# Optimization experiments

Hardware: AMD Instinct MI355X
Metric: run time of the kernel (lower is better)

The kernel has to match this reference:

```python
import jax, jax.numpy as jnp
import numpy as np

B, S, H = 2, 1024, 4544
NH, HD = 71, 64          # 71 query heads, head_dim 64, 1 shared kv head (multi-query)
THETA = 10000.0
NEG_INF = -1e9


def setup_inputs() -> dict:
    key = jax.random.key(0)
    k1, k2, k3 = jax.random.split(key, 3)
    hidden_states = jax.random.normal(k1, (B, S, H), dtype=jnp.float32)
    W_qkv = jax.random.normal(k2, (H, H + 2 * HD), dtype=jnp.float32) * 0.02
    W_dense = jax.random.normal(k3, (H, H), dtype=jnp.float32) * 0.02
    causal = jnp.tril(jnp.ones((S, S), dtype=bool))
    attention_mask = jnp.where(causal, 0.0, NEG_INF).astype(jnp.float32)[None, None]  # [1,1,S,S]
    position_ids = jnp.arange(S, dtype=jnp.int32)[None]  # [1,S]
    return {"hidden_states": hidden_states, "W_qkv": W_qkv, "W_dense": W_dense,
            "attention_mask": attention_mask, "position_ids": position_ids}


def _rope_cos_sin(position_ids):
    # HF FalconRotaryEmbedding: inv_freq over even dims, emb = cat(freqs, freqs)
    inv_freq = 1.0 / (THETA ** (jnp.arange(0, HD, 2, dtype=jnp.float32) / HD))
    freqs = position_ids.astype(jnp.float32)[..., None] * inv_freq  # [1,S,HD/2]
    emb = jnp.concatenate([freqs, freqs], axis=-1)                  # [1,S,HD]
    return jnp.cos(emb)[:, None], jnp.sin(emb)[:, None]             # [1,1,S,HD]


def _rotate_half(x):
    return jnp.concatenate([-x[..., HD // 2:], x[..., :HD // 2]], axis=-1)


def reference(hidden_states, W_qkv, W_dense, attention_mask, position_ids):
    # fused QKV projection (bias=False for Falcon-7B)
    fused = hidden_states @ W_qkv                       # [B,S,(NH+2)*HD]
    fused = fused.reshape(B, S, NH + 2, HD)
    q = jnp.transpose(fused[:, :, :NH], (0, 2, 1, 3))          # [B,NH,S,HD]
    k = jnp.transpose(fused[:, :, NH:NH + 1], (0, 2, 1, 3))    # [B,1,S,HD]
    v = jnp.transpose(fused[:, :, NH + 1:], (0, 2, 1, 3))      # [B,1,S,HD]

    cos, sin = _rope_cos_sin(position_ids)
    q = q * cos + _rotate_half(q) * sin
    k = k * cos + _rotate_half(k) * sin

    # scores: shared kv head broadcasts across the 71 query heads
    scores = jnp.matmul(q, jnp.swapaxes(k, -1, -2)) * (1.0 / np.sqrt(HD))  # [B,NH,S,S]
    probs = jax.nn.softmax(scores + attention_mask, axis=-1)
    attn = jnp.matmul(probs, v)                                            # [B,NH,S,HD]

    attn = jnp.transpose(attn, (0, 2, 1, 3)).reshape(B, S, NH * HD)
    return attn @ W_dense
```

## Files before the change

kernel.cpp:

```cpp
#include <hip/hip_runtime.h>

typedef unsigned short u16;
using f32x4  = __attribute__((ext_vector_type(4))) float;
using f32x16 = __attribute__((ext_vector_type(16))) float;
using s16x8  = __attribute__((ext_vector_type(8))) short;

static __device__ __forceinline__ u16 f2b(float f) {
  unsigned int u = __builtin_bit_cast(unsigned int, f);
  u = (u + 0x7fffu + ((u >> 16) & 1u)) >> 16;
  return (u16)u;
}
static __device__ __forceinline__ float b2f(u16 h) {
  unsigned int u = ((unsigned int)h) << 16;
  return __builtin_bit_cast(float, u);
}
static __device__ __forceinline__ unsigned int cvtpk(float lo, float hi) {
  unsigned int r;
  asm("v_cvt_pk_bf16_f32 %0, %1, %2" : "=v"(r) : "v"(lo), "v"(hi));
  return r;
}
static __device__ __forceinline__ void gload16(const void* g, void* l) {
  __builtin_amdgcn_global_load_lds(
      (const __attribute__((address_space(1))) void*)g,
      (__attribute__((address_space(3))) void*)l, 16, 0, 0);
}

__global__ __launch_bounds__(256) void conv_bf16(
    const float* __restrict__ in, u16* __restrict__ out, int n8)
{
  int i = blockIdx.x * 256 + threadIdx.x;
  if (i >= n8) return;
  float4 a = *(const float4*)(in + (size_t)i * 8);
  float4 b = *(const float4*)(in + (size_t)i * 8 + 4);
  __align__(16) u16 tmp[8] = {f2b(a.x), f2b(a.y), f2b(a.z), f2b(a.w),
                              f2b(b.x), f2b(b.y), f2b(b.z), f2b(b.w)};
  *(uint4*)(out + (size_t)i * 8) = *(const uint4*)tmp;
}

__global__ __launch_bounds__(256) void transpose_conv(
    const float* __restrict__ W, u16* __restrict__ Wt, int K, int N)
{
  __shared__ u16 tile[64][72];
  const int t = threadIdx.x;
  const int n0 = blockIdx.x * 64, k0 = blockIdx.y * 64;
  #pragma unroll
  for (int i = 0; i < 4; ++i) {
    int idx = i * 256 + t;
    int r = idx >> 4;
    int c = (idx & 15) << 2;
    float4 v = make_float4(0.f, 0.f, 0.f, 0.f);
    if (n0 + c < N) v = *(const float4*)(W + (size_t)(k0 + r) * N + n0 + c);
    tile[r][c + 0] = f2b(v.x);
    tile[r][c + 1] = f2b(v.y);
    tile[r][c + 2] = f2b(v.z);
    tile[r][c + 3] = f2b(v.w);
  }
  __syncthreads();
  #pragma unroll
  for (int i = 0; i < 2; ++i) {
    int idx = i * 256 + t;
    int rn = idx >> 3;
    int c8 = (idx & 7) << 3;
    __align__(16) u16 tmp[8];
    #pragma unroll
    for (int j = 0; j < 8; ++j) tmp[j] = tile[c8 + j][rn];
    *(uint4*)(Wt + (size_t)(n0 + rn) * K + k0 + c8) = *(const uint4*)tmp;
  }
}

template<bool OUT_BF16>
__global__ __launch_bounds__(256) void gemm_bt(
    const u16* __restrict__ A, const u16* __restrict__ B,
    void* __restrict__ Cptr, int M, int N, int K)
{
  __shared__ __align__(16) u16 aLds[128 * 32];
  __shared__ __align__(16) u16 bLds[128 * 32];

  const int t = threadIdx.x, lane = t & 63, w = t >> 6;
  const int lr = lane & 15, lg = lane >> 4;
  const int wr = w >> 1, wc = w & 1;
  const int m0 = blockIdx.y * 128, n0 = blockIdx.x * 128;

  const int srow = lane >> 2;
  const int skc  = (lane & 3) << 3;

  f32x4 acc[4][4] = {};

  const int nk = K >> 5;
  for (int kt = 0; kt < nk; ++kt) {
    const int k0 = kt << 5;
    __syncthreads();
    #pragma unroll
    for (int i = 0; i < 2; ++i) {
      int row = i * 64 + w * 16 + srow;
      gload16(A + (size_t)(m0 + row) * K + k0 + skc,
              (char*)aLds + i * 4096 + w * 1024);
      gload16(B + (size_t)(n0 + row) * K + k0 + skc,
              (char*)bLds + i * 4096 + w * 1024);
    }
    __syncthreads();
    s16x8 af[4], bf[4];
    #pragma unroll
    for (int m = 0; m < 4; ++m)
      af[m] = *(const s16x8*)(aLds + (wr * 64 + m * 16 + lr) * 32 + lg * 8);
    #pragma unroll
    for (int n = 0; n < 4; ++n)
      bf[n] = *(const s16x8*)(bLds + (wc * 64 + n * 16 + lr) * 32 + lg * 8);
    #pragma unroll
    for (int m = 0; m < 4; ++m)
      #pragma unroll
      for (int n = 0; n < 4; ++n)
        acc[m][n] = __builtin_amdgcn_mfma_f32_16x16x32_bf16(af[m], bf[n], acc[m][n], 0, 0, 0);
  }

  #pragma unroll
  for (int m = 0; m < 4; ++m) {
    int row = m0 + wr * 64 + m * 16 + lg * 4;
    #pragma unroll
    for (int n = 0; n < 4; ++n) {
      int col = n0 + wc * 64 + n * 16 + lr;
      if (col < N) {
        #pragma unroll
        for (int r = 0; r < 4; ++r) {
          if constexpr (OUT_BF16)
            ((u16*)Cptr)[(size_t)(row + r) * N + col] = f2b(acc[m][n][r]);
          else
            ((float*)Cptr)[(size_t)(row + r) * N + col] = acc[m][n][r];
        }
      }
    }
  }
}

__global__ __launch_bounds__(256) void rope_extract(
    const u16* __restrict__ fused, const int* __restrict__ pos_ids,
    u16* __restrict__ q, u16* __restrict__ kx, u16* __restrict__ vT)
{
  const int t   = threadIdx.x;
  const int row = blockIdx.x * 4 + (t >> 6);
  const int d   = t & 63;
  const int b   = row >> 10, s = row & 1023;
  const float p = (float)pos_ids[s];
  const float inv = exp2f(-0.41524101186092029f * (float)(d & 31));
  float sn, cs;
  sincosf(p * inv, &sn, &cs);
  const float sgn = (d < 32) ? -1.f : 1.f;
  const int dp = (d + 32) & 63;
  const u16* base = fused + (size_t)row * 4672;

  for (int h = 0; h < 71; ++h) {
    float x  = b2f(base[h * 64 + d]);
    float xp = b2f(base[h * 64 + dp]);
    q[((size_t)(b * 71 + h) * 1024 + s) * 64 + d] = f2b(x * cs + sgn * xp * sn);
  }
  {
    float x  = b2f(base[71 * 64 + d]);
    float xp = b2f(base[71 * 64 + dp]);
    kx[((size_t)b * 1024 + s) * 64 + d] = f2b(x * cs + sgn * xp * sn);
  }
  vT[((size_t)b * 64 + d) * 1024 + s] = base[72 * 64 + d];
}

__global__ __launch_bounds__(128) void attn_kernel(
    const u16* __restrict__ q, const u16* __restrict__ kx,
    const u16* __restrict__ vT, u16* __restrict__ attnO)
{
  const int t = threadIdx.x, lane = t & 63, w = t >> 6;
  const int lq  = lane & 31;
  const int hi  = lane >> 5;
  const int hi4 = hi << 2;
  const int pair = blockIdx.x, h = blockIdx.y, b = blockIdx.z;
  const int qt = w ? (31 - pair) : pair;
  const int q0 = qt * 32;

  const u16* qbase = q + ((size_t)(b * 71 + h) * 1024 + q0 + lq) * 64 + hi * 8;
  s16x8 qf[4];
  #pragma unroll
  for (int kt = 0; kt < 4; ++kt) qf[kt] = *(const s16x8*)(qbase + kt * 16);

  f32x16 o0 = {}, o1 = {};
  float m = -1e30f, l = 0.f;

  const u16* kbase  = kx + ((size_t)b * 1024 + lq) * 64 + hi * 8;
  const u16* vbase0 = vT + ((size_t)b * 64 + lq) * 1024 + hi * 8;
  const u16* vbase1 = vbase0 + 32 * 1024;

  for (int it = 0; it <= qt; ++it) {
    const int kv0 = it * 32;
    s16x8 kf[4];
    #pragma unroll
    for (int kt = 0; kt < 4; ++kt)
      kf[kt] = *(const s16x8*)(kbase + (size_t)kv0 * 64 + kt * 16);
    s16x8 v00 = *(const s16x8*)(vbase0 + kv0);
    s16x8 v01 = *(const s16x8*)(vbase0 + kv0 + 16);
    s16x8 v10 = *(const s16x8*)(vbase1 + kv0);
    s16x8 v11 = *(const s16x8*)(vbase1 + kv0 + 16);

    f32x16 sa = {}, sb = {};
    sa = __builtin_amdgcn_mfma_f32_32x32x16_bf16(kf[0], qf[0], sa, 0, 0, 0);
    sb = __builtin_amdgcn_mfma_f32_32x32x16_bf16(kf[1], qf[1], sb, 0, 0, 0);
    sa = __builtin_amdgcn_mfma_f32_32x32x16_bf16(kf[2], qf[2], sa, 0, 0, 0);
    sb = __builtin_amdgcn_mfma_f32_32x32x16_bf16(kf[3], qf[3], sb, 0, 0, 0);

    float s[16];
    float pmax = -1e30f;
    if (it == qt) {
      #pragma unroll
      for (int r = 0; r < 16; ++r) {
        int R = (r & 3) + ((r >> 2) << 3) + hi4;
        s[r] = (R > lq) ? -1e30f : (sa[r] + sb[r]) * 0.125f;
        pmax = fmaxf(pmax, s[r]);
      }
    } else {
      #pragma unroll
      for (int r = 0; r < 16; ++r) {
        s[r] = (sa[r] + sb[r]) * 0.125f;
        pmax = fmaxf(pmax, s[r]);
      }
    }
    pmax = fmaxf(pmax, __shfl_xor(pmax, 32));

    if (!__all(pmax <= m + 8.f)) {
      float mn = fmaxf(m, pmax);
      float corr = __expf(m - mn);
      m = mn;
      l *= corr;
      #pragma unroll
      for (int r = 0; r < 16; ++r) {
        float c2 = __shfl(corr, (r & 3) + ((r >> 2) << 3) + hi4);
        o0[r] *= c2; o1[r] *= c2;
      }
    }

    float p[16], sum = 0.f;
    #pragma unroll
    for (int r = 0; r < 16; ++r) { p[r] = __expf(s[r] - m); sum += p[r]; }
    sum += __shfl_xor(sum, 32);
    l += sum;

    unsigned int a0 = cvtpk(p[0], p[1]),   a1 = cvtpk(p[2], p[3]);
    unsigned int b0 = cvtpk(p[4], p[5]),   b1 = cvtpk(p[6], p[7]);
    asm("v_permlane32_swap_b32 %0, %1" : "+v"(a0), "+v"(b0));
    asm("v_permlane32_swap_b32 %0, %1" : "+v"(a1), "+v"(b1));
    unsigned int c0 = cvtpk(p[8], p[9]),   c1 = cvtpk(p[10], p[11]);
    unsigned int d0 = cvtpk(p[12], p[13]), d1 = cvtpk(p[14], p[15]);
    asm("v_permlane32_swap_b32 %0, %1" : "+v"(c0), "+v"(d0));
    asm("v_permlane32_swap_b32 %0, %1" : "+v"(c1), "+v"(d1));
    union { unsigned int wd[4]; s16x8 v; } palo, pahi;
    palo.wd[0] = a0; palo.wd[1] = a1; palo.wd[2] = b0; palo.wd[3] = b1;
    pahi.wd[0] = c0; pahi.wd[1] = c1; pahi.wd[2] = d0; pahi.wd[3] = d1;

    o0 = __builtin_amdgcn_mfma_f32_32x32x16_bf16(palo.v, v00, o0, 0, 0, 0);
    o0 = __builtin_amdgcn_mfma_f32_32x32x16_bf16(pahi.v, v01, o0, 0, 0, 0);
    o1 = __builtin_amdgcn_mfma_f32_32x32x16_bf16(palo.v, v10, o1, 0, 0, 0);
    o1 = __builtin_amdgcn_mfma_f32_32x32x16_bf16(pahi.v, v11, o1, 0, 0, 0);
  }

  float linv = 1.f / l;
  #pragma unroll
  for (int r = 0; r < 16; ++r) {
    int R = (r & 3) + ((r >> 2) << 3) + hi4;
    float c2 = __shfl(linv, R);
    size_t base = ((size_t)(b * 1024 + q0 + R) * 71 + h) * 64;
    attnO[base + lq]      = f2b(o0[r] * c2);
    attnO[base + 32 + lq] = f2b(o1[r] * c2);
  }
}

extern "C" void kernel_launch(void* const* d_in, const int* in_sizes, int n_in,
                              void* d_out, int out_size, void* d_ws, size_t ws_size,
                              hipStream_t stream) {
  const float* hidden = (const float*)d_in[0];
  const float* Wqkv   = (const float*)d_in[1];
  const float* Wdense = (const float*)d_in[2];
  const int*   pos    = (const int*)d_in[4];
  float* out = (float*)d_out;

  char* wsp = (char*)d_ws;
  u16* Wt    = (u16*)(wsp);
  u16* A1    = (u16*)(wsp + 43040768);
  u16* fused = (u16*)(wsp + 43040768 + 18612224);
  u16* kws   = (u16*)(wsp + 43040768 + 18612224 + 19136512);
  u16* vws   = (u16*)(wsp + 43040768 + 18612224 + 19136512 + 262144);
  u16* qws   = A1;
  u16* attnw = fused;

  conv_bf16<<<4544, 256, 0, stream>>>(hidden, A1, 2048 * 4544 / 8);
  transpose_conv<<<dim3(74, 71), 256, 0, stream>>>(Wqkv, Wt, 4544, 4672);
  gemm_bt<true><<<dim3(37, 16), 256, 0, stream>>>(A1, Wt, fused, 2048, 4672, 4544);
  rope_extract<<<512, 256, 0, stream>>>(fused, pos, qws, kws, vws);
  transpose_conv<<<dim3(72, 71), 256, 0, stream>>>(Wdense, Wt, 4544, 4544);
  attn_kernel<<<dim3(16, 71, 2), 128, 0, stream>>>(qws, kws, vws, attnw);
  gemm_bt<false><<<dim3(36, 16), 256, 0, stream>>>(attnw, Wt, out, 2048, 4544, 4544);
}
```

Before: 462.1 us.

## Replace GEMM with 256x256 double-buffered, pipelined MFMA kernel with block swizzle

Replaces the 128x128 single-buffered GEMM with a 256x256-tile, 512-thread kernel. It uses double-buffered LDS with 64-wide K steps, prefetches the next stage with global_load_lds, interleaves barriers and s_setprio around MFMA groups, and remaps block IDs with an XCD-style swizzle. The goal is more operand reuse per tile and overlap of memory loads with compute in both projection GEMMs. The risks are higher register and LDS pressure, a small grid (152/144 blocks) that may not cover all CUs, and a larger padded weight buffer.

```diff
diff --git a/kernel.cpp b/kernel.cpp
--- a/kernel.cpp
+++ b/kernel.cpp
@@ -69,53 +69,106 @@
 }
 
 template<bool OUT_BF16>
-__global__ __launch_bounds__(256) void gemm_bt(
+__global__ __launch_bounds__(512, 2) void gemm256(
     const u16* __restrict__ A, const u16* __restrict__ B,
-    void* __restrict__ Cptr, int M, int N, int K)
-{
-  __shared__ __align__(16) u16 aLds[128 * 32];
-  __shared__ __align__(16) u16 bLds[128 * 32];
+    void* __restrict__ Cptr, int M, int N, int K, int NB)
+{
+  __shared__ __align__(16) u16 sA[2][2][256 * 32];
+  __shared__ __align__(16) u16 sB[2][2][256 * 32];
 
   const int t = threadIdx.x, lane = t & 63, w = t >> 6;
   const int lr = lane & 15, lg = lane >> 4;
-  const int wr = w >> 1, wc = w & 1;
-  const int m0 = blockIdx.y * 128, n0 = blockIdx.x * 128;
-
-  const int srow = lane >> 2;
+  const int wr = w >> 2, wc = w & 3;
+
+  int bid = blockIdx.x;
+  int q = gridDim.x >> 3;
+  int swz = (bid & 7) * q + (bid >> 3);
+  const int m0 = (swz / NB) * 256, n0 = (swz % NB) * 256;
+
+  const int srow = w * 32 + (lane >> 2);
   const int skc  = (lane & 3) << 3;
-
-  f32x4 acc[4][4] = {};
-
-  const int nk = K >> 5;
+  const u16* Ast = A + (size_t)(m0 + srow) * K + skc;
+  const u16* Bst = B + (size_t)(n0 + srow) * K + skc;
+  const int ldsoff = w * 2048;
+
+  f32x4 acc[8][4] = {};
+  const int nk = K >> 6;
+
+#define STAGEU(tt, ks) do {                                                   \
+    int bp_ = (tt) & 1; size_t kc_ = (size_t)(tt) * 64 + (size_t)(ks) * 32;   \
+    gload16(Ast + kc_,                 (char*)&sA[bp_][ks][0] + ldsoff);      \
+    gload16(Ast + kc_ + 16 * (size_t)K,(char*)&sA[bp_][ks][0] + ldsoff+1024); \
+    gload16(Bst + kc_,                 (char*)&sB[bp_][ks][0] + ldsoff);      \
+    gload16(Bst + kc_ + 16 * (size_t)K,(char*)&sB[bp_][ks][0] + ldsoff+1024); \
+  } while (0)
+
+#define LOADA(rh, ks, cur) do {                                               \
+    const u16* ap_ = &sA[cur][ks][0] + ((wr*128 + (rh)*64 + lr) * 32) + lg*8; \
+    af[0] = *(const s16x8*)(ap_);                                             \
+    af[1] = *(const s16x8*)(ap_ + 16*32);                                     \
+    af[2] = *(const s16x8*)(ap_ + 32*32);                                     \
+    af[3] = *(const s16x8*)(ap_ + 48*32);                                     \
+  } while (0)
+
+#define LOADB(ks, cur) do {                                                   \
+    const u16* bp2_ = &sB[cur][ks][0] + ((wc*64 + lr) * 32) + lg*8;           \
+    bf[0] = *(const s16x8*)(bp2_);                                            \
+    bf[1] = *(const s16x8*)(bp2_ + 16*32);                                    \
+    bf[2] = *(const s16x8*)(bp2_ + 32*32);                                    \
+    bf[3] = *(const s16x8*)(bp2_ + 48*32);                                    \
+  } while (0)
+
+#define MFMAQ(rh) do {                                                        \
+    __builtin_amdgcn_s_setprio(1);                                            \
+    _Pragma("unroll")                                                         \
+    for (int m_ = 0; m_ < 4; ++m_)                                            \
+      _Pragma("unroll")                                                       \
+      for (int n_ = 0; n_ < 4; ++n_)                                          \
+        acc[(rh)*4 + m_][n_] = __builtin_amdgcn_mfma_f32_16x16x32_bf16(       \
+            af[m_], bf[n_], acc[(rh)*4 + m_][n_], 0, 0, 0);                   \
+    __builtin_amdgcn_s_setprio(0);                                            \
+  } while (0)
+
+  STAGEU(0, 0);
+  STAGEU(0, 1);
+  if (nk > 1) STAGEU(1, 0);
+  asm volatile("s_waitcnt vmcnt(8)" ::: "memory");
+  __builtin_amdgcn_s_barrier();
+
   for (int kt = 0; kt < nk; ++kt) {
-    const int k0 = kt << 5;
-    __syncthreads();
-    #pragma unroll
-    for (int i = 0; i < 2; ++i) {
-      int row = i * 64 + w * 16 + srow;
-      gload16(A + (size_t)(m0 + row) * K + k0 + skc,
-              (char*)aLds + i * 4096 + w * 1024);
-      gload16(B + (size_t)(n0 + row) * K + k0 + skc,
-              (char*)bLds + i * 4096 + w * 1024);
-    }
-    __syncthreads();
+    const int cur = kt & 1;
     s16x8 af[4], bf[4];
-    #pragma unroll
-    for (int m = 0; m < 4; ++m)
-      af[m] = *(const s16x8*)(aLds + (wr * 64 + m * 16 + lr) * 32 + lg * 8);
-    #pragma unroll
-    for (int n = 0; n < 4; ++n)
-      bf[n] = *(const s16x8*)(bLds + (wc * 64 + n * 16 + lr) * 32 + lg * 8);
-    #pragma unroll
-    for (int m = 0; m < 4; ++m)
-      #pragma unroll
-      for (int n = 0; n < 4; ++n)
-        acc[m][n] = __builtin_amdgcn_mfma_f32_16x16x32_bf16(af[m], bf[n], acc[m][n], 0, 0, 0);
-  }
-
-  #pragma unroll
-  for (int m = 0; m < 4; ++m) {
-    int row = m0 + wr * 64 + m * 16 + lg * 4;
+    if (kt + 1 < nk) STAGEU(kt + 1, 1);
+    LOADA(0, 0, cur); LOADB(0, cur);
+    __builtin_amdgcn_s_barrier();
+    MFMAQ(0);
+    __builtin_amdgcn_s_barrier();
+    LOADA(1, 0, cur);
+    __builtin_amdgcn_s_barrier();
+    MFMAQ(1);
+    if (kt + 1 < nk) asm volatile("s_waitcnt vmcnt(8)" ::: "memory");
+    else             asm volatile("s_waitcnt vmcnt(0)" ::: "memory");
+    __builtin_amdgcn_s_barrier();
+    if (kt + 2 < nk) STAGEU(kt + 2, 0);
+    LOADA(0, 1, cur); LOADB(1, cur);
+    __builtin_amdgcn_s_barrier();
+    MFMAQ(0);
+    __builtin_amdgcn_s_barrier();
+    LOADA(1, 1, cur);
+    __builtin_amdgcn_s_barrier();
+    MFMAQ(1);
+    if (kt + 2 < nk)      asm volatile("s_waitcnt vmcnt(8)" ::: "memory");
+    else if (kt + 1 < nk) asm volatile("s_waitcnt vmcnt(4)" ::: "memory");
+    __builtin_amdgcn_s_barrier();
+  }
+#undef STAGEU
+#undef LOADA
+#undef LOADB
+#undef MFMAQ
+
+  #pragma unroll
+  for (int mm = 0; mm < 8; ++mm) {
+    int row = m0 + wr * 128 + (mm >> 2) * 64 + (mm & 3) * 16 + lg * 4;
     #pragma unroll
     for (int n = 0; n < 4; ++n) {
       int col = n0 + wc * 64 + n * 16 + lr;
@@ -123,9 +176,9 @@
         #pragma unroll
         for (int r = 0; r < 4; ++r) {
           if constexpr (OUT_BF16)
-            ((u16*)Cptr)[(size_t)(row + r) * N + col] = f2b(acc[m][n][r]);
+            ((u16*)Cptr)[(size_t)(row + r) * N + col] = f2b(acc[mm][n][r]);
           else
-            ((float*)Cptr)[(size_t)(row + r) * N + col] = acc[m][n][r];
+            ((float*)Cptr)[(size_t)(row + r) * N + col] = acc[mm][n][r];
         }
       }
     }
@@ -278,18 +331,18 @@
 
   char* wsp = (char*)d_ws;
   u16* Wt    = (u16*)(wsp);
-  u16* A1    = (u16*)(wsp + 43040768);
-  u16* fused = (u16*)(wsp + 43040768 + 18612224);
-  u16* kws   = (u16*)(wsp + 43040768 + 18612224 + 19136512);
-  u16* vws   = (u16*)(wsp + 43040768 + 18612224 + 19136512 + 262144);
+  u16* A1    = (u16*)(wsp + 44208128);
+  u16* fused = (u16*)(wsp + 44208128 + 18612224);
+  u16* kws   = (u16*)(wsp + 44208128 + 18612224 + 19136512);
+  u16* vws   = (u16*)(wsp + 44208128 + 18612224 + 19136512 + 262144);
   u16* qws   = A1;
   u16* attnw = fused;
 
   conv_bf16<<<4544, 256, 0, stream>>>(hidden, A1, 2048 * 4544 / 8);
-  transpose_conv<<<dim3(74, 71), 256, 0, stream>>>(Wqkv, Wt, 4544, 4672);
-  gemm_bt<true><<<dim3(37, 16), 256, 0, stream>>>(A1, Wt, fused, 2048, 4672, 4544);
+  transpose_conv<<<dim3(76, 71), 256, 0, stream>>>(Wqkv, Wt, 4544, 4672);
+  gemm256<true><<<152, 512, 0, stream>>>(A1, Wt, fused, 2048, 4672, 4544, 19);
   rope_extract<<<512, 256, 0, stream>>>(fused, pos, qws, kws, vws);
   transpose_conv<<<dim3(72, 71), 256, 0, stream>>>(Wdense, Wt, 4544, 4544);
   attn_kernel<<<dim3(16, 71, 2), 128, 0, stream>>>(qws, kws, vws, attnw);
-  gemm_bt<false><<<dim3(36, 16), 256, 0, stream>>>(attnw, Wt, out, 2048, 4544, 4544);
-}
+  gemm256<false><<<144, 512, 0, stream>>>(attnw, Wt, out, 2048, 4544, 4544, 18);
+}
```

Result: slower. 565.4 us (+22.3%).

## Fuse RoPE and Q/K/V extraction into QKV GEMM epilogue, swizzle block order

Applied to the files above, without the earlier changes.

Drops the separate rope_extract kernel. The QKV GEMM epilogue now applies rotary embedding directly from the fp32 accumulators and writes q, k and transposed v in their final layouts, so the bf16 fused intermediate is never written and re-read. Both GEMMs also switch to a 1D grid with a block-index swizzle meant to improve L2 reuse of A/B tiles. The trade-off is a heavier epilogue with scattered 2-byte stores (especially the strided vT writes) and fast __sincosf, which is less accurate than sincosf.

```diff
diff --git a/kernel.cpp b/kernel.cpp
--- a/kernel.cpp
+++ b/kernel.cpp
@@ -68,10 +68,13 @@
   }
 }
 
-template<bool OUT_BF16>
+template<int MODE>
 __global__ __launch_bounds__(256) void gemm_bt(
     const u16* __restrict__ A, const u16* __restrict__ B,
-    void* __restrict__ Cptr, int M, int N, int K)
+    float* __restrict__ Cptr,
+    u16* __restrict__ qo, u16* __restrict__ ko, u16* __restrict__ vo,
+    const int* __restrict__ pos,
+    int M, int N, int K, int NBX)
 {
   __shared__ __align__(16) u16 aLds[128 * 32];
   __shared__ __align__(16) u16 bLds[128 * 32];
@@ -79,7 +82,11 @@
   const int t = threadIdx.x, lane = t & 63, w = t >> 6;
   const int lr = lane & 15, lg = lane >> 4;
   const int wr = w >> 1, wc = w & 1;
-  const int m0 = blockIdx.y * 128, n0 = blockIdx.x * 128;
+
+  const int bid = blockIdx.x;
+  const int qq  = gridDim.x >> 3;
+  const int swz = (bid & 7) * qq + (bid >> 3);
+  const int m0 = (swz / NBX) * 128, n0 = (swz % NBX) * 128;
 
   const int srow = lane >> 2;
   const int skc  = (lane & 3) << 3;
@@ -113,52 +120,58 @@
         acc[m][n] = __builtin_amdgcn_mfma_f32_16x16x32_bf16(af[m], bf[n], acc[m][n], 0, 0, 0);
   }
 
-  #pragma unroll
-  for (int m = 0; m < 4; ++m) {
-    int row = m0 + wr * 64 + m * 16 + lg * 4;
-    #pragma unroll
-    for (int n = 0; n < 4; ++n) {
-      int col = n0 + wc * 64 + n * 16 + lr;
-      if (col < N) {
-        #pragma unroll
-        for (int r = 0; r < 4; ++r) {
-          if constexpr (OUT_BF16)
-            ((u16*)Cptr)[(size_t)(row + r) * N + col] = f2b(acc[m][n][r]);
-          else
-            ((float*)Cptr)[(size_t)(row + r) * N + col] = acc[m][n][r];
+  if constexpr (MODE == 0) {
+    #pragma unroll
+    for (int m = 0; m < 4; ++m) {
+      int row = m0 + wr * 64 + m * 16 + lg * 4;
+      #pragma unroll
+      for (int n = 0; n < 4; ++n) {
+        int col = n0 + wc * 64 + n * 16 + lr;
+        if (col < N) {
+          #pragma unroll
+          for (int r = 0; r < 4; ++r)
+            Cptr[(size_t)(row + r) * N + col] = acc[m][n][r];
         }
       }
     }
-  }
-}
-
-__global__ __launch_bounds__(256) void rope_extract(
-    const u16* __restrict__ fused, const int* __restrict__ pos_ids,
-    u16* __restrict__ q, u16* __restrict__ kx, u16* __restrict__ vT)
-{
-  const int t   = threadIdx.x;
-  const int row = blockIdx.x * 4 + (t >> 6);
-  const int d   = t & 63;
-  const int b   = row >> 10, s = row & 1023;
-  const float p = (float)pos_ids[s];
-  const float inv = exp2f(-0.41524101186092029f * (float)(d & 31));
-  float sn, cs;
-  sincosf(p * inv, &sn, &cs);
-  const float sgn = (d < 32) ? -1.f : 1.f;
-  const int dp = (d + 32) & 63;
-  const u16* base = fused + (size_t)row * 4672;
-
-  for (int h = 0; h < 71; ++h) {
-    float x  = b2f(base[h * 64 + d]);
-    float xp = b2f(base[h * 64 + dp]);
-    q[((size_t)(b * 71 + h) * 1024 + s) * 64 + d] = f2b(x * cs + sgn * xp * sn);
-  }
-  {
-    float x  = b2f(base[71 * 64 + d]);
-    float xp = b2f(base[71 * 64 + dp]);
-    kx[((size_t)b * 1024 + s) * 64 + d] = f2b(x * cs + sgn * xp * sn);
-  }
-  vT[((size_t)b * 64 + d) * 1024 + s] = base[72 * 64 + d];
+  } else {
+    const int h = (n0 + wc * 64) >> 6;
+    if (h > 72) return;
+    const float inv0 = exp2f(-0.41524101186092029f * (float)lr);
+    const float inv1 = exp2f(-0.41524101186092029f * (float)(16 + lr));
+    #pragma unroll
+    for (int m = 0; m < 4; ++m) {
+      #pragma unroll
+      for (int r = 0; r < 4; ++r) {
+        int row = m0 + wr * 64 + m * 16 + lg * 4 + r;
+        int b = row >> 10, s = row & 1023;
+        if (h == 72) {
+          #pragma unroll
+          for (int n = 0; n < 4; ++n) {
+            int d = n * 16 + lr;
+            vo[((size_t)b * 64 + d) * 1024 + s] = f2b(acc[m][n][r]);
+          }
+        } else {
+          float p = (float)pos[s];
+          float sn0, cs0, sn1, cs1;
+          __sincosf(p * inv0, &sn0, &cs0);
+          __sincosf(p * inv1, &sn1, &cs1);
+          #pragma unroll
+          for (int n = 0; n < 4; ++n) {
+            float cs  = (n & 1) ? cs1 : cs0;
+            float sn  = (n & 1) ? sn1 : sn0;
+            float sgn = (n < 2) ? -1.f : 1.f;
+            float val = acc[m][n][r] * cs + sgn * acc[m][n ^ 2][r] * sn;
+            int d = n * 16 + lr;
+            if (h < 71)
+              qo[((size_t)(b * 71 + h) * 1024 + s) * 64 + d] = f2b(val);
+            else
+              ko[((size_t)b * 1024 + s) * 64 + d] = f2b(val);
+          }
+        }
+      }
+    }
+  }
 }
 
 __global__ __launch_bounds__(128) void attn_kernel(
@@ -279,17 +292,17 @@
   char* wsp = (char*)d_ws;
   u16* Wt    = (u16*)(wsp);
   u16* A1    = (u16*)(wsp + 43040768);
-  u16* fused = (u16*)(wsp + 43040768 + 18612224);
-  u16* kws   = (u16*)(wsp + 43040768 + 18612224 + 19136512);
-  u16* vws   = (u16*)(wsp + 43040768 + 18612224 + 19136512 + 262144);
-  u16* qws   = A1;
-  u16* attnw = fused;
+  u16* qws   = (u16*)(wsp + 43040768 + 18612224);
+  u16* kws   = (u16*)(wsp + 43040768 + 18612224 + 18612224);
+  u16* vws   = (u16*)(wsp + 43040768 + 18612224 + 18612224 + 262144);
+  u16* attnw = A1;
 
   conv_bf16<<<4544, 256, 0, stream>>>(hidden, A1, 2048 * 4544 / 8);
   transpose_conv<<<dim3(74, 71), 256, 0, stream>>>(Wqkv, Wt, 4544, 4672);
-  gemm_bt<true><<<dim3(37, 16), 256, 0, stream>>>(A1, Wt, fused, 2048, 4672, 4544);
-  rope_extract<<<512, 256, 0, stream>>>(fused, pos, qws, kws, vws);
+  gemm_bt<2><<<592, 256, 0, stream>>>(A1, Wt, nullptr, qws, kws, vws, pos,
+                                      2048, 4672, 4544, 37);
   transpose_conv<<<dim3(72, 71), 256, 0, stream>>>(Wdense, Wt, 4544, 4544);
   attn_kernel<<<dim3(16, 71, 2), 128, 0, stream>>>(qws, kws, vws, attnw);
-  gemm_bt<false><<<dim3(36, 16), 256, 0, stream>>>(attnw, Wt, out, 2048, 4544, 4544);
-}
+  gemm_bt<0><<<576, 256, 0, stream>>>(attnw, Wt, out, nullptr, nullptr, nullptr,
+                                      nullptr, 2048, 4544, 4544, 36);
+}
```

New measurement: 448.7 us. -2.9%, faster.
